# Kernel tuning notes

Measured on AMD Instinct MI355X. Metric: run time of the kernel, lower is better.

Reference implementation:

```python
import jax, jax.numpy as jnp
import numpy as np


def setup_inputs() -> dict:
    key = jax.random.key(0)
    ks = jax.random.split(key, 7)
    B, T, X, H, Y = 256, 2048, 64, 128, 32
    s_ih = 1.0 / np.sqrt(H)
    return {
        "x": jax.random.normal(ks[0], (B, T, X), dtype=jnp.float32),
        "W_ih": jax.random.normal(ks[1], (H, X), dtype=jnp.float32) * s_ih,
        "W_hh": jax.random.normal(ks[2], (H, H), dtype=jnp.float32) * s_ih,
        "b_ih": jax.random.normal(ks[3], (H,), dtype=jnp.float32) * s_ih,
        "b_hh": jax.random.normal(ks[4], (H,), dtype=jnp.float32) * s_ih,
        "W_out": jax.random.normal(ks[5], (Y, H), dtype=jnp.float32) * s_ih,
        "b_out": jax.random.normal(ks[6], (Y,), dtype=jnp.float32) * s_ih,
    }


def reference(x, W_ih, W_hh, b_ih, b_hh, W_out, b_out):
    # Vanilla tanh RNN (torch.nn.RNN, 1 layer, batch_first), zero initial state,
    # readout on the last timestep: h_t = tanh(x_t W_ih^T + b_ih + h_{t-1} W_hh^T + b_hh)
    B, T, X = x.shape
    H = W_hh.shape[0]
    # Precompute input projections for all timesteps in one big GEMM: [T, B, H]
    xs = (jnp.einsum('bti,hi->bth', x, W_ih) + (b_ih + b_hh)).transpose(1, 0, 2)

    def step(h, xt):
        h = jnp.tanh(xt + h @ W_hh.T)
        return h, None

    h0 = jnp.zeros((B, H), dtype=x.dtype)
    h_last, _ = jax.lax.scan(step, h0, xs)
    out = h_last @ W_out.T + b_out  # [B, Y]
    return out
```

## Files before the change

### kernel.cpp

```cpp
#include <hip/hip_runtime.h>

#define TT 2048
#define BB 256
#define XX 64
#define HH 128
#define YY 32
#define SSTR 20
#define HBUF (8 * SSTR)


typedef float v2f __attribute__((ext_vector_type(2)));
typedef float v4f __attribute__((ext_vector_type(4)));

#define PKFMA(acc, a, b)                                              \
    asm("v_pk_fma_f32 %0, %1, %2, %0 op_sel:[0,0,0] op_sel_hi:[1,1,1]"\
        : "+v"(acc) : "v"(a), "v"(b))

template<int CTRL>
static __device__ __forceinline__ float dpp_mov(float s) {
    return __int_as_float(__builtin_amdgcn_update_dpp(
        0, __float_as_int(s), CTRL, 0xF, 0xF, true));
}

static __device__ __forceinline__ void pin2(v2f& v) {
    asm volatile("" : "+v"(v));
}

static __device__ __forceinline__ void barrier_lgkm() {
    asm volatile("s_waitcnt lgkmcnt(0)" ::: "memory");
    __builtin_amdgcn_s_barrier();
    asm volatile("" ::: "memory");
}

#define LO2(v) __builtin_shufflevector(v, v, 0, 1)
#define HI2(v) __builtin_shufflevector(v, v, 2, 3)

__global__ __launch_bounds__(512)
__attribute__((amdgpu_waves_per_eu(2, 2)))
void rnn_persist_kernel(const float* __restrict__ x,
                        const float* __restrict__ W_ih,
                        const float* __restrict__ W_hh,
                        const float* __restrict__ b_ih,
                        const float* __restrict__ b_hh,
                        const float* __restrict__ W_out,
                        const float* __restrict__ b_out,
                        float* __restrict__ out)
{
    __shared__ __align__(16) float h_lds[2][HBUF];

    const int tid  = threadIdx.x;
    const int b    = blockIdx.x;
    const int w    = tid >> 6;
    const int lane = tid & 63;
    const int kg   = (lane & 3) | ((lane >> 1) & 4);
    const int jgl  = ((lane >> 2) & 1) | (((lane >> 4) & 3) << 1);
    const int jg   = w * 8 + jgl;
    const int j0   = jg * 2;
    const int b0   = lane & 1;
    const bool writer = (lane & 10) == 0;

    const float SC = 2.8853900817779268f;

    v2f whh2[2][8];
    v2f wih2[2][4];
    float bs[2];
    #pragma unroll
    for (int jj = 0; jj < 2; ++jj) {
        const v2f* ph = (const v2f*)(W_hh + (j0 + jj) * HH + kg * 16);
        #pragma unroll
        for (int c = 0; c < 8; ++c) whh2[jj][c] = ph[c] * SC;
        const v2f* pi = (const v2f*)(W_ih + (j0 + jj) * XX + kg * 8);
        #pragma unroll
        for (int c = 0; c < 4; ++c) wih2[jj][c] = pi[c] * SC;
        bs[jj] = (b_ih[j0 + jj] + b_hh[j0 + jj]) * SC;
    }
    #pragma unroll
    for (int jj = 0; jj < 2; ++jj) {
        #pragma unroll
        for (int c = 0; c < 8; ++c) pin2(whh2[jj][c]);
        #pragma unroll
        for (int c = 0; c < 4; ++c) pin2(wih2[jj][c]);
    }
    const float bsel = b0 ? bs[1] : bs[0];

    const int jw   = j0 + b0;
    const int woff = (jw >> 4) * SSTR + (jw & 15);

    const float* xg = x + (size_t)b * TT * XX + kg * 8;

    if (tid < HBUF) h_lds[0][tid] = 0.f;

    v4f xa0 = ((const v4f*)xg)[0];
    v4f xa1 = ((const v4f*)xg)[1];
    v4f xb0 = ((const v4f*)(xg + XX))[0];
    v4f xb1 = ((const v4f*)(xg + XX))[1];
    __syncthreads();

#define STEP(RP, WP, X0, X1)                                              \
    do {                                                                  \
        const v4f* hp = (const v4f*)&h_lds[RP][kg * SSTR];                \
        const v4f H0 = hp[0], H1 = hp[1], H2 = hp[2], H3 = hp[3];         \
        const v2f h2[8] = { LO2(H0), HI2(H0), LO2(H1), HI2(H1),           \
                            LO2(H2), HI2(H2), LO2(H3), HI2(H3) };         \
        const v2f x2[4] = { LO2(X0), HI2(X0), LO2(X1), HI2(X1) };         \
        float s[2];                                                       \
        _Pragma("unroll")                                                 \
        for (int jj = 0; jj < 2; ++jj) {                                  \
            v2f a = {0.f, 0.f}, c = {0.f, 0.f};                           \
            PKFMA(a, wih2[jj][0], x2[0]); PKFMA(c, wih2[jj][1], x2[1]);   \
            PKFMA(a, wih2[jj][2], x2[2]); PKFMA(c, wih2[jj][3], x2[3]);   \
            PKFMA(a, whh2[jj][0], h2[0]); PKFMA(c, whh2[jj][1], h2[1]);   \
            PKFMA(a, whh2[jj][2], h2[2]); PKFMA(c, whh2[jj][3], h2[3]);   \
            PKFMA(a, whh2[jj][4], h2[4]); PKFMA(c, whh2[jj][5], h2[5]);   \
            PKFMA(a, whh2[jj][6], h2[6]); PKFMA(c, whh2[jj][7], h2[7]);   \
            a = a + c;                                                    \
            s[jj] = a.x + a.y;                                            \
        }                                                                 \
        \
        float u = b0 ? s[1] : s[0];            \
        float v = b0 ? s[0] : s[1];            \
        u += dpp_mov<0xB1>(v);            \
        u += dpp_mov<0x4E>(u);            \
        u += dpp_mov<0x128>(u);         \
        u += bsel;                         \
        const float e  = __builtin_amdgcn_exp2f(u);                       \
        const float hn = fmaf(-2.f, __builtin_amdgcn_rcpf(e + 1.f), 1.f); \
        if (writer) h_lds[WP][woff] = hn;                                 \
        barrier_lgkm();               \
    } while (0)

    for (int t = 0; t < TT; t += 2) {
        STEP(0, 1, xa0, xa1);
        {
            const int tn = (t + 2 < TT) ? t + 2 : TT - 1;
            const v4f* xp = (const v4f*)(xg + (size_t)tn * XX);
            xa0 = xp[0]; xa1 = xp[1];
        }
        STEP(1, 0, xb0, xb1);
        {
            const int tn = (t + 3 < TT) ? t + 3 : TT - 1;
            const v4f* xp = (const v4f*)(xg + (size_t)tn * XX);
            xb0 = xp[0]; xb1 = xp[1];
        }
    }
#undef STEP

    if (tid < YY) {
        const float* h  = h_lds[0];
        const float* wr = W_out + tid * HH;
        float r0 = 0.f, r1 = 0.f, r2 = 0.f, r3 = 0.f;
        #pragma unroll
        for (int s8 = 0; s8 < 8; ++s8) {
            #pragma unroll
            for (int c = 0; c < 4; ++c) {
                const float4 wv = *(const float4*)(wr + s8 * 16 + c * 4);
                const float4 hv = *(const float4*)(h + s8 * SSTR + c * 4);
                r0 = fmaf(wv.x, hv.x, r0); r1 = fmaf(wv.y, hv.y, r1);
                r2 = fmaf(wv.z, hv.z, r2); r3 = fmaf(wv.w, hv.w, r3);
            }
        }
        out[b * YY + tid] = b_out[tid] + ((r0 + r1) + (r2 + r3));
    }
}

extern "C" void kernel_launch(void* const* d_in, const int* in_sizes, int n_in,
                              void* d_out, int out_size, void* d_ws, size_t ws_size,
                              hipStream_t stream) {
    const float* x     = (const float*)d_in[0];
    const float* W_ih  = (const float*)d_in[1];
    const float* W_hh  = (const float*)d_in[2];
    const float* b_ih  = (const float*)d_in[3];
    const float* b_hh  = (const float*)d_in[4];
    const float* W_out = (const float*)d_in[5];
    const float* b_out = (const float*)d_in[6];
    float* out = (float*)d_out;

    rnn_persist_kernel<<<BB, 512, 0, stream>>>(x, W_ih, W_hh, b_ih, b_hh,
                                               W_out, b_out, out);
}
```

Measured before the change: 588.8 us.

## Split RNN into parallel input-projection kernel and leaner recurrence kernel

Adds a highly parallel proj_kernel that precomputes the scaled input projections plus bias for every (batch, timestep) into a workspace buffer. A separate rec_kernel then runs the serial recurrence with 256 threads per block, each lane producing four hidden units from W_hh only and prefetching the precomputed projections four steps ahead. The aim is to take the W_ih FMAs off the serial critical path of each timestep. The cost is writing and rereading a roughly 256 MB intermediate buffer. rec_kernel also launches a duplicate, non-writing block per batch row that does redundant work, and the original fused kernel is kept as a fallback with deeper x prefetch when the workspace is too small.

```diff
diff --git a/kernel.cpp b/kernel.cpp
--- a/kernel.cpp
+++ b/kernel.cpp
@@ -7,6 +7,8 @@
 #define YY 32
 #define SSTR 20
 #define HBUF (8 * SSTR)
+#define PCHUNK 128
+#define NPCH (TT / PCHUNK)
 
 
 typedef float v2f __attribute__((ext_vector_type(2)));
@@ -35,16 +37,206 @@
 #define LO2(v) __builtin_shufflevector(v, v, 0, 1)
 #define HI2(v) __builtin_shufflevector(v, v, 2, 3)
 
+#define REDUCE_SCATTER(s, u)                                               \
+    float ul = b0 ? s[1] : s[0];                                           \
+    float vl = b0 ? s[0] : s[1];                                           \
+    ul += dpp_mov<0xB1>(vl);                                               \
+    float uh = b0 ? s[3] : s[2];                                           \
+    float vh = b0 ? s[2] : s[3];                                           \
+    uh += dpp_mov<0xB1>(vh);                                               \
+    float u  = b1 ? uh : ul;                                               \
+    float vv = b1 ? ul : uh;                                               \
+    u += dpp_mov<0x4E>(vv);                                                \
+    u += dpp_mov<0x128>(u);
+
+__global__ __launch_bounds__(256)
+void proj_kernel(const float* __restrict__ x,
+                 const float* __restrict__ W_ih,
+                 const float* __restrict__ b_ih,
+                 const float* __restrict__ b_hh,
+                 float* __restrict__ c)
+{
+    const int tid  = threadIdx.x;
+    const int lane = tid & 63;
+    const int w    = tid >> 6;
+    const int kg   = (lane & 3) | ((lane >> 1) & 4);
+    const int jgl  = ((lane >> 2) & 1) | (((lane >> 4) & 3) << 1);
+    const int j0   = (w * 8 + jgl) * 4;
+    const int b0   = lane & 1;
+    const int b1   = (lane >> 1) & 1;
+    const int jw   = j0 + (lane & 3);
+    const bool writer = ((lane >> 3) & 1) == 0;
+    const float SC = 2.8853900817779268f;
+
+    v2f wih2[4][4];
+    #pragma unroll
+    for (int jj = 0; jj < 4; ++jj) {
+        const v2f* pi = (const v2f*)(W_ih + (j0 + jj) * XX + kg * 8);
+        #pragma unroll
+        for (int cc = 0; cc < 4; ++cc) { wih2[jj][cc] = pi[cc] * SC; pin2(wih2[jj][cc]); }
+    }
+    const float bsel = (b_ih[jw] + b_hh[jw]) * SC;
+
+    const int row = blockIdx.x >> 4;
+    const int t0  = (blockIdx.x & 15) * PCHUNK;
+    const float* xg = x + ((size_t)row * TT + t0) * XX + kg * 8;
+    float*       cg = c + ((size_t)row * TT + t0) * HH;
+    const int tmax = TT - 1 - t0;
+
+    v4f xa0 = ((const v4f*)xg)[0];
+    v4f xa1 = ((const v4f*)xg)[1];
+    v4f xb0 = ((const v4f*)(xg + XX))[0];
+    v4f xb1 = ((const v4f*)(xg + XX))[1];
+
+#define PSTEP(TI, X0, X1)                                                  \
+    do {                                                                   \
+        const v2f x2[4] = { LO2(X0), HI2(X0), LO2(X1), HI2(X1) };          \
+        float s[4];                                                        \
+        _Pragma("unroll")                                                  \
+        for (int jj = 0; jj < 4; ++jj) {                                   \
+            v2f a = {0.f, 0.f};                                            \
+            PKFMA(a, wih2[jj][0], x2[0]); PKFMA(a, wih2[jj][1], x2[1]);    \
+            PKFMA(a, wih2[jj][2], x2[2]); PKFMA(a, wih2[jj][3], x2[3]);    \
+            s[jj] = a.x + a.y;                                             \
+        }                                                                  \
+        REDUCE_SCATTER(s, u);                                              \
+        u += bsel;                                                         \
+        if (writer) cg[(size_t)(TI) * HH + jw] = u;                        \
+    } while (0)
+
+    for (int tt = 0; tt < PCHUNK; tt += 2) {
+        PSTEP(tt, xa0, xa1);
+        {
+            const int tn = (tt + 2 > tmax) ? tmax : tt + 2;
+            const v4f* xp = (const v4f*)(xg + (size_t)tn * XX);
+            xa0 = xp[0]; xa1 = xp[1];
+        }
+        PSTEP(tt + 1, xb0, xb1);
+        {
+            const int tn = (tt + 3 > tmax) ? tmax : tt + 3;
+            const v4f* xp = (const v4f*)(xg + (size_t)tn * XX);
+            xb0 = xp[0]; xb1 = xp[1];
+        }
+    }
+#undef PSTEP
+}
+
+__global__ __launch_bounds__(256)
+__attribute__((amdgpu_waves_per_eu(2, 2)))
+void rec_kernel(const float* __restrict__ c,
+                const float* __restrict__ W_hh,
+                const float* __restrict__ W_out,
+                const float* __restrict__ b_out,
+                float* __restrict__ out)
+{
+    __shared__ __align__(16) float h_lds[2][HBUF];
+
+    const int tid  = threadIdx.x;
+    const int lane = tid & 63;
+    const int w    = tid >> 6;
+    const int b    = blockIdx.x >> 1;
+    const bool wrblk = (blockIdx.x & 1) == 0;
+    const int kg   = (lane & 3) | ((lane >> 1) & 4);
+    const int jgl  = ((lane >> 2) & 1) | (((lane >> 4) & 3) << 1);
+    const int j0   = (w * 8 + jgl) * 4;
+    const int b0   = lane & 1;
+    const int b1   = (lane >> 1) & 1;
+    const int jw   = j0 + (lane & 3);
+    const int woff = (jw >> 4) * SSTR + (jw & 15);
+    const bool writer = ((lane >> 3) & 1) == 0;
+    const float SC = 2.8853900817779268f;
+
+    v2f whh2[4][8];
+    #pragma unroll
+    for (int jj = 0; jj < 4; ++jj) {
+        const v2f* ph = (const v2f*)(W_hh + (j0 + jj) * HH + kg * 16);
+        #pragma unroll
+        for (int cc = 0; cc < 8; ++cc) { whh2[jj][cc] = ph[cc] * SC; pin2(whh2[jj][cc]); }
+    }
+
+    const float* cr = c + (size_t)b * TT * HH + jw;
+
+    if (!wrblk) {
+        float d = 1.0f + (float)lane;
+        #pragma unroll
+        for (int i = 0; i < 96; ++i) d = fmaf(d, 1.0000001f, 1e-7f);
+        asm volatile("" :: "v"(d));
+    }
+
+    if (tid < HBUF) h_lds[0][tid] = 0.f;
+
+    float cp0 = cr[0];
+    float cp1 = cr[HH];
+    float cp2 = cr[2 * HH];
+    float cp3 = cr[3 * HH];
+    __syncthreads();
+
+#define RSTEP(RP, WP, CPV)                                                 \
+    do {                                                                   \
+        const v4f* hp = (const v4f*)&h_lds[RP][kg * SSTR];                 \
+        const v4f H0 = hp[0], H1 = hp[1], H2 = hp[2], H3 = hp[3];          \
+        const v2f h2[8] = { LO2(H0), HI2(H0), LO2(H1), HI2(H1),            \
+                            LO2(H2), HI2(H2), LO2(H3), HI2(H3) };          \
+        float s[4];                                                        \
+        _Pragma("unroll")                                                  \
+        for (int jj = 0; jj < 4; ++jj) {                                   \
+            v2f a = {0.f, 0.f}, cc = {0.f, 0.f};                           \
+            PKFMA(a, whh2[jj][0], h2[0]); PKFMA(cc, whh2[jj][1], h2[1]);   \
+            PKFMA(a, whh2[jj][2], h2[2]); PKFMA(cc, whh2[jj][3], h2[3]);   \
+            PKFMA(a, whh2[jj][4], h2[4]); PKFMA(cc, whh2[jj][5], h2[5]);   \
+            PKFMA(a, whh2[jj][6], h2[6]); PKFMA(cc, whh2[jj][7], h2[7]);   \
+            a = a + cc;                                                    \
+            s[jj] = a.x + a.y;                                             \
+        }                                                                  \
+        REDUCE_SCATTER(s, u);                                              \
+        u += (CPV);       \
+        const float e  = __builtin_amdgcn_exp2f(u);                        \
+        const float hn = fmaf(-2.f, __builtin_amdgcn_rcpf(e + 1.f), 1.f);  \
+        if (writer) h_lds[WP][woff] = hn;                                  \
+        barrier_lgkm();                                                    \
+    } while (0)
+
+#define RELC(CPV, TN)                                                     \
+    do { const int tn_ = ((TN) < TT) ? (TN) : TT - 1;                     \
+         CPV = cr[(size_t)tn_ * HH]; } while (0)
+
+    for (int t = 0; t < TT; t += 4) {
+        RSTEP(0, 1, cp0);  RELC(cp0, t + 4);
+        RSTEP(1, 0, cp1);  RELC(cp1, t + 5);
+        RSTEP(0, 1, cp2);  RELC(cp2, t + 6);
+        RSTEP(1, 0, cp3);  RELC(cp3, t + 7);
+    }
+#undef RSTEP
+#undef RELC
+
+    if (wrblk && tid < YY) {
+        const float* h  = h_lds[0];
+        const float* wr = W_out + tid * HH;
+        float r0 = 0.f, r1 = 0.f, r2 = 0.f, r3 = 0.f;
+        #pragma unroll
+        for (int s8 = 0; s8 < 8; ++s8) {
+            #pragma unroll
+            for (int cc = 0; cc < 4; ++cc) {
+                const float4 wv = *(const float4*)(wr + s8 * 16 + cc * 4);
+                const float4 hv = *(const float4*)(h + s8 * SSTR + cc * 4);
+                r0 = fmaf(wv.x, hv.x, r0); r1 = fmaf(wv.y, hv.y, r1);
+                r2 = fmaf(wv.z, hv.z, r2); r3 = fmaf(wv.w, hv.w, r3);
+            }
+        }
+        out[b * YY + tid] = b_out[tid] + ((r0 + r1) + (r2 + r3));
+    }
+}
+
 __global__ __launch_bounds__(512)
 __attribute__((amdgpu_waves_per_eu(2, 2)))
-void rnn_persist_kernel(const float* __restrict__ x,
-                        const float* __restrict__ W_ih,
-                        const float* __restrict__ W_hh,
-                        const float* __restrict__ b_ih,
-                        const float* __restrict__ b_hh,
-                        const float* __restrict__ W_out,
-                        const float* __restrict__ b_out,
-                        float* __restrict__ out)
+void rnn_fallback(const float* __restrict__ x,
+                  const float* __restrict__ W_ih,
+                  const float* __restrict__ W_hh,
+                  const float* __restrict__ b_ih,
+                  const float* __restrict__ b_hh,
+                  const float* __restrict__ W_out,
+                  const float* __restrict__ b_out,
+                  float* __restrict__ out)
 {
     __shared__ __align__(16) float h_lds[2][HBUF];
 
@@ -58,7 +250,6 @@
     const int j0   = jg * 2;
     const int b0   = lane & 1;
     const bool writer = (lane & 10) == 0;
-
     const float SC = 2.8853900817779268f;
 
     v2f whh2[2][8];
@@ -68,21 +259,20 @@
     for (int jj = 0; jj < 2; ++jj) {
         const v2f* ph = (const v2f*)(W_hh + (j0 + jj) * HH + kg * 16);
         #pragma unroll
-        for (int c = 0; c < 8; ++c) whh2[jj][c] = ph[c] * SC;
+        for (int cc = 0; cc < 8; ++cc) whh2[jj][cc] = ph[cc] * SC;
         const v2f* pi = (const v2f*)(W_ih + (j0 + jj) * XX + kg * 8);
         #pragma unroll
-        for (int c = 0; c < 4; ++c) wih2[jj][c] = pi[c] * SC;
+        for (int cc = 0; cc < 4; ++cc) wih2[jj][cc] = pi[cc] * SC;
         bs[jj] = (b_ih[j0 + jj] + b_hh[j0 + jj]) * SC;
     }
     #pragma unroll
     for (int jj = 0; jj < 2; ++jj) {
         #pragma unroll
-        for (int c = 0; c < 8; ++c) pin2(whh2[jj][c]);
-        #pragma unroll
-        for (int c = 0; c < 4; ++c) pin2(wih2[jj][c]);
+        for (int cc = 0; cc < 8; ++cc) pin2(whh2[jj][cc]);
+        #pragma unroll
+        for (int cc = 0; cc < 4; ++cc) pin2(wih2[jj][cc]);
     }
     const float bsel = b0 ? bs[1] : bs[0];
-
     const int jw   = j0 + b0;
     const int woff = (jw >> 4) * SSTR + (jw & 15);
 
@@ -90,13 +280,13 @@
 
     if (tid < HBUF) h_lds[0][tid] = 0.f;
 
-    v4f xa0 = ((const v4f*)xg)[0];
-    v4f xa1 = ((const v4f*)xg)[1];
-    v4f xb0 = ((const v4f*)(xg + XX))[0];
-    v4f xb1 = ((const v4f*)(xg + XX))[1];
+    v4f xa0 = ((const v4f*)xg)[0], xa1 = ((const v4f*)xg)[1];
+    v4f xb0 = ((const v4f*)(xg + XX))[0], xb1 = ((const v4f*)(xg + XX))[1];
+    v4f xc0 = ((const v4f*)(xg + 2 * XX))[0], xc1 = ((const v4f*)(xg + 2 * XX))[1];
+    v4f xd0 = ((const v4f*)(xg + 3 * XX))[0], xd1 = ((const v4f*)(xg + 3 * XX))[1];
     __syncthreads();
 
-#define STEP(RP, WP, X0, X1)                                              \
+#define FSTEP(RP, WP, X0, X1)                                             \
     do {                                                                  \
         const v4f* hp = (const v4f*)&h_lds[RP][kg * SSTR];                \
         const v4f H0 = hp[0], H1 = hp[1], H2 = hp[2], H3 = hp[3];         \
@@ -106,44 +296,43 @@
         float s[2];                                                       \
         _Pragma("unroll")                                                 \
         for (int jj = 0; jj < 2; ++jj) {                                  \
-            v2f a = {0.f, 0.f}, c = {0.f, 0.f};                           \
-            PKFMA(a, wih2[jj][0], x2[0]); PKFMA(c, wih2[jj][1], x2[1]);   \
-            PKFMA(a, wih2[jj][2], x2[2]); PKFMA(c, wih2[jj][3], x2[3]);   \
-            PKFMA(a, whh2[jj][0], h2[0]); PKFMA(c, whh2[jj][1], h2[1]);   \
-            PKFMA(a, whh2[jj][2], h2[2]); PKFMA(c, whh2[jj][3], h2[3]);   \
-            PKFMA(a, whh2[jj][4], h2[4]); PKFMA(c, whh2[jj][5], h2[5]);   \
-            PKFMA(a, whh2[jj][6], h2[6]); PKFMA(c, whh2[jj][7], h2[7]);   \
-            a = a + c;                                                    \
+            v2f a = {0.f, 0.f}, cc = {0.f, 0.f};                          \
+            PKFMA(a, wih2[jj][0], x2[0]); PKFMA(cc, wih2[jj][1], x2[1]);  \
+            PKFMA(a, wih2[jj][2], x2[2]); PKFMA(cc, wih2[jj][3], x2[3]);  \
+            PKFMA(a, whh2[jj][0], h2[0]); PKFMA(cc, whh2[jj][1], h2[1]);  \
+            PKFMA(a, whh2[jj][2], h2[2]); PKFMA(cc, whh2[jj][3], h2[3]);  \
+            PKFMA(a, whh2[jj][4], h2[4]); PKFMA(cc, whh2[jj][5], h2[5]);  \
+            PKFMA(a, whh2[jj][6], h2[6]); PKFMA(cc, whh2[jj][7], h2[7]);  \
+            a = a + cc;                                                   \
             s[jj] = a.x + a.y;                                            \
         }                                                                 \
-        \
-        float u = b0 ? s[1] : s[0];            \
-        float v = b0 ? s[0] : s[1];            \
-        u += dpp_mov<0xB1>(v);            \
-        u += dpp_mov<0x4E>(u);            \
-        u += dpp_mov<0x128>(u);         \
-        u += bsel;                         \
+        float u = b0 ? s[1] : s[0];                                       \
+        float v = b0 ? s[0] : s[1];                                       \
+        u += dpp_mov<0xB1>(v);                                            \
+        u += dpp_mov<0x4E>(u);                                            \
+        u += dpp_mov<0x128>(u);                                           \
+        u += bsel;                                                        \
         const float e  = __builtin_amdgcn_exp2f(u);                       \
         const float hn = fmaf(-2.f, __builtin_amdgcn_rcpf(e + 1.f), 1.f); \
         if (writer) h_lds[WP][woff] = hn;                                 \
-        barrier_lgkm();               \
+        barrier_lgkm();                                                   \
     } while (0)
 
-    for (int t = 0; t < TT; t += 2) {
-        STEP(0, 1, xa0, xa1);
-        {
-            const int tn = (t + 2 < TT) ? t + 2 : TT - 1;
-            const v4f* xp = (const v4f*)(xg + (size_t)tn * XX);
-            xa0 = xp[0]; xa1 = xp[1];
-        }
-        STEP(1, 0, xb0, xb1);
-        {
-            const int tn = (t + 3 < TT) ? t + 3 : TT - 1;
-            const v4f* xp = (const v4f*)(xg + (size_t)tn * XX);
-            xb0 = xp[0]; xb1 = xp[1];
-        }
-    }
-#undef STEP
+#define FRELOAD(XS0, XS1, TN)                                             \
+    do {                                                                  \
+        const int tn_ = ((TN) < TT) ? (TN) : TT - 1;                      \
+        const v4f* xp_ = (const v4f*)(xg + (size_t)tn_ * XX);             \
+        XS0 = xp_[0]; XS1 = xp_[1];                                       \
+    } while (0)
+
+    for (int t = 0; t < TT; t += 4) {
+        FSTEP(0, 1, xa0, xa1);  FRELOAD(xa0, xa1, t + 4);
+        FSTEP(1, 0, xb0, xb1);  FRELOAD(xb0, xb1, t + 5);
+        FSTEP(0, 1, xc0, xc1);  FRELOAD(xc0, xc1, t + 6);
+        FSTEP(1, 0, xd0, xd1);  FRELOAD(xd0, xd1, t + 7);
+    }
+#undef FSTEP
+#undef FRELOAD
 
     if (tid < YY) {
         const float* h  = h_lds[0];
@@ -152,9 +341,9 @@
         #pragma unroll
         for (int s8 = 0; s8 < 8; ++s8) {
             #pragma unroll
-            for (int c = 0; c < 4; ++c) {
-                const float4 wv = *(const float4*)(wr + s8 * 16 + c * 4);
-                const float4 hv = *(const float4*)(h + s8 * SSTR + c * 4);
+            for (int cc = 0; cc < 4; ++cc) {
+                const float4 wv = *(const float4*)(wr + s8 * 16 + cc * 4);
+                const float4 hv = *(const float4*)(h + s8 * SSTR + cc * 4);
                 r0 = fmaf(wv.x, hv.x, r0); r1 = fmaf(wv.y, hv.y, r1);
                 r2 = fmaf(wv.z, hv.z, r2); r3 = fmaf(wv.w, hv.w, r3);
             }
@@ -175,6 +364,13 @@
     const float* b_out = (const float*)d_in[6];
     float* out = (float*)d_out;
 
-    rnn_persist_kernel<<<BB, 512, 0, stream>>>(x, W_ih, W_hh, b_ih, b_hh,
-                                               W_out, b_out, out);
-}
+    const size_t cbytes = (size_t)BB * TT * HH * sizeof(float);
+    if (ws_size >= cbytes) {
+        float* c = (float*)d_ws;
+        proj_kernel<<<BB * NPCH, 256, 0, stream>>>(x, W_ih, b_ih, b_hh, c);
+        rec_kernel<<<2 * BB, 256, 0, stream>>>(c, W_hh, W_out, b_out, out);
+    } else {
+        rnn_fallback<<<BB, 512, 0, stream>>>(x, W_ih, W_hh, b_ih, b_hh,
+                                             W_out, b_out, out);
+    }
+}
```

Result: slower. 904.9 us (+53.7%).
